# Optimization experiments

Hardware: AMD Instinct MI355X
Metric: run time of the kernel (lower is better)

## Reference

```python
import jax, jax.numpy as jnp
import numpy as np

THRESHOLD = 0.5
NEG_POS_RATIO = 3
ALPHA = 1.0
B, N_OBJ, N_PRIORS, N_CLASSES = 64, 32, 8732, 81


def xy_to_cxcy(xy):
    return jnp.concatenate([(xy[..., :2] + xy[..., 2:]) / 2.0, xy[..., 2:] - xy[..., :2]], axis=-1)


def cxcy_to_gcxgcy(cxcy, priors):
    return jnp.concatenate([
        (cxcy[..., :2] - priors[..., :2]) / (priors[..., 2:] / 10.0),
        jnp.log(cxcy[..., 2:] / priors[..., 2:]) * 5.0,
    ], axis=-1)


def jaccard(a, b):
    # a: [n,4], b: [m,4], both interpreted as (x1,y1,x2,y2) -- the original code
    # passes priors_cxcy directly (faithfully reproduced here).
    lt = jnp.maximum(a[:, None, :2], b[None, :, :2])
    rb = jnp.minimum(a[:, None, 2:], b[None, :, 2:])
    inter = jnp.prod(jnp.clip(rb - lt, 0.0, None), axis=-1)          # [n,m]
    area_a = jnp.prod(a[:, 2:] - a[:, :2], axis=-1)                  # [n]
    area_b = jnp.prod(b[:, 2:] - b[:, :2], axis=-1)                  # [m]
    return inter / (area_a[:, None] + area_b[None, :] - inter)


def _match(boxes_i, labels_i, priors_cxcy):
    # boxes_i: [n_obj,4] xy, labels_i: [n_obj] int, priors_cxcy: [n_priors,4]
    n_obj = boxes_i.shape[0]
    ov = jaccard(boxes_i, priors_cxcy)                               # [n_obj, n_priors]
    ov_for_prior = ov.max(axis=0)                                    # [n_priors]
    obj_for_prior = ov.argmax(axis=0)                                # [n_priors]
    prior_for_obj = ov.argmax(axis=1)                                # [n_obj]
    obj_for_prior = obj_for_prior.at[prior_for_obj].set(jnp.arange(n_obj))
    ov_for_prior = ov_for_prior.at[prior_for_obj].set(1.0)
    lab = labels_i[obj_for_prior]
    lab = jnp.where(ov_for_prior < THRESHOLD, 0, lab)                # background
    true_locs = cxcy_to_gcxgcy(xy_to_cxcy(boxes_i[obj_for_prior]), priors_cxcy)
    return true_locs, lab


def setup_inputs() -> dict:
    key = jax.random.key(0)
    k1, k2, k3, k4, k5, k6, k7 = jax.random.split(key, 7)
    predicted_locs = jax.random.normal(k1, (B, N_PRIORS, 4), dtype=jnp.float32)
    predicted_scores = jax.random.normal(k2, (B, N_PRIORS, N_CLASSES), dtype=jnp.float32)
    # valid gt boxes in xy form, inside [0,1]
    cxy = 0.15 + 0.7 * jax.random.uniform(k3, (B, N_OBJ, 2))
    wh = 0.05 + 0.25 * jax.random.uniform(k4, (B, N_OBJ, 2))
    boxes = jnp.clip(jnp.concatenate([cxy - wh / 2, cxy + wh / 2], axis=-1), 0.0, 1.0).astype(jnp.float32)
    labels = jax.random.randint(k5, (B, N_OBJ), 1, N_CLASSES)        # foreground classes
    # priors: cx,cy small, w,h large so that treating (cx,cy,w,h) as xy (as the
    # original code does in jaccard) still yields positive areas
    p_cxy = 0.4 * jax.random.uniform(k6, (N_PRIORS, 2))
    p_wh = 0.5 + 0.5 * jax.random.uniform(k7, (N_PRIORS, 2))
    priors_cxcy = jnp.concatenate([p_cxy, p_wh], axis=-1).astype(jnp.float32)
    return {
        "predicted_locs": predicted_locs,
        "predicted_scores": predicted_scores,
        "boxes": boxes,
        "labels": labels,
        "priors_cxcy": priors_cxcy,
    }


def multibox_loss(predicted_locs, predicted_scores, boxes, labels, priors_cxcy):
    n_priors = priors_cxcy.shape[0]
    true_locs, true_classes = jax.vmap(_match, in_axes=(0, 0, None))(boxes, labels, priors_cxcy)
    pos = true_classes != 0                                          # [B, n_priors]
    pos_f = pos.astype(predicted_locs.dtype)
    n_pos = pos.sum(axis=1)                                          # [B]
    n_pos_total = n_pos.sum().astype(jnp.float32)
    # nn.L1Loss(): mean over the 4 coords of positive priors
    loc_loss = (jnp.abs(predicted_locs - true_locs) * pos_f[..., None]).sum() / (n_pos_total * 4.0)
    # per-prior cross entropy
    logp = jax.nn.log_softmax(predicted_scores, axis=-1)             # [B,P,C]
    ce = -jnp.take_along_axis(logp, true_classes[..., None], axis=-1)[..., 0]  # [B,P]
    conf_pos = (ce * pos_f).sum()
    ce_neg = jnp.where(pos, 0.0, ce)
    ce_neg_sorted = -jnp.sort(-ce_neg, axis=1)                       # descending
    ranks = jnp.arange(n_priors)[None, :]
    hard = (ranks < (NEG_POS_RATIO * n_pos)[:, None]).astype(ce.dtype)
    conf_hard_neg = (ce_neg_sorted * hard).sum()
    conf_loss = (conf_hard_neg + conf_pos) / n_pos_total
    return conf_loss + ALPHA * loc_loss


def reference(predicted_locs, predicted_scores, boxes, labels, priors_cxcy):
    return multibox_loss(predicted_locs, predicted_scores, boxes, labels, priors_cxcy)
```

## Files before the change

kernel.cpp:

```cpp
#include <hip/hip_runtime.h>
#include <math.h>
#include <stdint.h>

#define BATCH 64
#define N_OBJ 32
#define NP 8732
#define NC 81
#define THRESH 0.5f


__device__ __forceinline__ float iou_box_prior(float x1, float y1, float x2, float y2,
                                               float areaA, float4 pr, float areaB) {
    float iw = fminf(x2, pr.z) - fmaxf(x1, pr.x); iw = fmaxf(iw, 0.f);
    float ih = fminf(y2, pr.w) - fmaxf(y1, pr.y); ih = fmaxf(ih, 0.f);
    float inter = iw * ih;
    return inter / (areaA + areaB - inter);
}

__global__ void k_match_prior(const float* __restrict__ boxes,
                              const float* __restrict__ priors,
                              float* __restrict__ ovp, int* __restrict__ objp,
                              int* __restrict__ n_pos, float* __restrict__ scal) {
    int i = blockIdx.y;
    int t = threadIdx.x;
    if (blockIdx.x == 0 && i == 0) {
        if (t < BATCH) n_pos[t] = 0;
        if (t < 3) scal[t] = 0.f;
    }
    __shared__ float bx[N_OBJ * 4];
    if (t < N_OBJ * 4) bx[t] = boxes[i * N_OBJ * 4 + t];
    __syncthreads();
    int p = blockIdx.x * blockDim.x + t;
    if (p >= NP) return;
    float4 pr = ((const float4*)priors)[p];
    float areaB = (pr.z - pr.x) * (pr.w - pr.y);
    float best = -1.0f; int bestj = 0;
    #pragma unroll
    for (int j = 0; j < N_OBJ; ++j) {
        float x1 = bx[j * 4 + 0], y1 = bx[j * 4 + 1], x2 = bx[j * 4 + 2], y2 = bx[j * 4 + 3];
        float areaA = (x2 - x1) * (y2 - y1);
        float v = iou_box_prior(x1, y1, x2, y2, areaA, pr, areaB);
        if (v > best) { best = v; bestj = j; }
    }
    ovp[i * NP + p] = best;
    objp[i * NP + p] = bestj;
}

__global__ void k_match_obj(const float* __restrict__ boxes,
                            const float* __restrict__ priors,
                            int* __restrict__ pfo) {
    int j = blockIdx.x, i = blockIdx.y;
    const float* bp = boxes + (i * N_OBJ + j) * 4;
    float x1 = bp[0], y1 = bp[1], x2 = bp[2], y2 = bp[3];
    float areaA = (x2 - x1) * (y2 - y1);
    float best = -1.f; int bestp = NP;
    for (int p = threadIdx.x; p < NP; p += blockDim.x) {
        float4 pr = ((const float4*)priors)[p];
        float areaB = (pr.z - pr.x) * (pr.w - pr.y);
        float v = iou_box_prior(x1, y1, x2, y2, areaA, pr, areaB);
        if (v > best) { best = v; bestp = p; }
    }
    __shared__ float sv[256];
    __shared__ int   si[256];
    int t = threadIdx.x;
    sv[t] = best; si[t] = bestp;
    __syncthreads();
    for (int s = 128; s > 0; s >>= 1) {
        if (t < s) {
            float v2 = sv[t + s]; int i2 = si[t + s];
            if (v2 > sv[t] || (v2 == sv[t] && i2 < si[t])) { sv[t] = v2; si[t] = i2; }
        }
        __syncthreads();
    }
    if (t == 0) pfo[i * N_OBJ + j] = si[0];
}

__global__ void k_force(const int* __restrict__ pfo,
                        float* __restrict__ ovp, int* __restrict__ objp) {
    int i = blockIdx.x * blockDim.x + threadIdx.x;
    if (i >= BATCH) return;
    for (int j = 0; j < N_OBJ; ++j) {
        int p = pfo[i * N_OBJ + j];
        objp[i * NP + p] = j;
        ovp[i * NP + p] = 1.0f;
    }
}

__global__ void __launch_bounds__(256)
k_ce(const float* __restrict__ scores,
     const float* __restrict__ plocs,
     const float* __restrict__ boxes,
     const int*   __restrict__ labels,
     const float* __restrict__ priors,
     const float* __restrict__ ovp,
     const int*   __restrict__ objp,
     float* __restrict__ ce_neg,
     int* __restrict__ n_pos, float* __restrict__ scal) {
    int i = blockIdx.y;
    int p = blockIdx.x * 256 + threadIdx.x;
    if (p >= NP) return;
    int gi = i * NP + p;

    int   obj = objp[gi];
    float ov  = ovp[gi];
    int   lab = (ov < THRESH) ? 0 : labels[i * N_OBJ + obj];

    const float* row = scores + (size_t)gi * NC;
    float slab = row[lab];

    float x[NC];
    #pragma unroll
    for (int e = 0; e < NC; ++e) x[e] = row[e];

    float m0 = x[0], m1 = x[1], m2 = x[2], m3 = x[3];
    #pragma unroll
    for (int e = 4; e + 3 < NC; e += 4) {
        m0 = fmaxf(m0, x[e + 0]);
        m1 = fmaxf(m1, x[e + 1]);
        m2 = fmaxf(m2, x[e + 2]);
        m3 = fmaxf(m3, x[e + 3]);
    }
    m0 = fmaxf(m0, x[NC - 1]);
    float m = fmaxf(fmaxf(m0, m1), fmaxf(m2, m3));

    float s0 = 0.f, s1 = 0.f, s2 = 0.f, s3 = 0.f;
    #pragma unroll
    for (int e = 0; e + 3 < NC; e += 4) {
        s0 += __expf(x[e + 0] - m);
        s1 += __expf(x[e + 1] - m);
        s2 += __expf(x[e + 2] - m);
        s3 += __expf(x[e + 3] - m);
    }
    s0 += __expf(x[NC - 1] - m);
    float s = (s0 + s1) + (s2 + s3);

    float lse = m + __logf(s);
    float ce = lse - slab;

    if (lab != 0) {
        atomicAdd(&n_pos[i], 1);
        atomicAdd(&scal[0], ce);
        const float* bp = boxes + (i * N_OBJ + obj) * 4;
        float bx1 = bp[0], by1 = bp[1], bx2 = bp[2], by2 = bp[3];
        float bcx = (bx1 + bx2) * 0.5f, bcy = (by1 + by2) * 0.5f;
        float bw = bx2 - bx1, bh = by2 - by1;
        float4 pr = ((const float4*)priors)[p];
        float g0 = (bcx - pr.x) / (pr.z / 10.0f);
        float g1 = (bcy - pr.y) / (pr.w / 10.0f);
        float g2 = logf(bw / pr.z) * 5.0f;
        float g3 = logf(bh / pr.w) * 5.0f;
        const float* pl = plocs + (size_t)gi * 4;
        float ll = fabsf(pl[0] - g0) + fabsf(pl[1] - g1)
                 + fabsf(pl[2] - g2) + fabsf(pl[3] - g3);
        atomicAdd(&scal[2], ll);
        ce_neg[gi] = 0.f;
    } else {
        ce_neg[gi] = ce;
    }
}

__global__ void __launch_bounds__(256)
k_topk(const float* __restrict__ ce_neg,
       const int* __restrict__ n_pos, float* __restrict__ scal) {
    int i = blockIdx.x;
    int t = threadIdx.x;
    float x[35];
    #pragma unroll
    for (int j = 0; j < 35; ++j) {
        int p = t + j * 256;
        x[j] = (p < NP) ? ce_neg[i * NP + p] : 0.f;
    }
    int k = 3 * n_pos[i];
    if (k > NP) k = NP;
    if (k <= 0) return;

    __shared__ int   cnt_s[4];
    __shared__ float sum_s[4];
    unsigned lo = 0u, hi = 0x7F800001u;
    while (hi - lo > 1u) {
        unsigned mid = lo + ((hi - lo) >> 1);
        int c = 0;
        #pragma unroll
        for (int j = 0; j < 35; ++j) c += (__float_as_uint(x[j]) >= mid) ? 1 : 0;
        #pragma unroll
        for (int off = 32; off; off >>= 1) c += __shfl_xor(c, off);
        if ((t & 63) == 0) cnt_s[t >> 6] = c;
        __syncthreads();
        int total = cnt_s[0] + cnt_s[1] + cnt_s[2] + cnt_s[3];
        __syncthreads();
        if (total >= k) lo = mid; else hi = mid;
    }
    float vk = __uint_as_float(lo);

    float s = 0.f; int c = 0;
    #pragma unroll
    for (int j = 0; j < 35; ++j) {
        float v = x[j];
        if (v > vk) { s += v; c++; }
    }
    #pragma unroll
    for (int off = 32; off; off >>= 1) { s += __shfl_xor(s, off); c += __shfl_xor(c, off); }
    if ((t & 63) == 0) { sum_s[t >> 6] = s; cnt_s[t >> 6] = c; }
    __syncthreads();
    if (t == 0) {
        float st = sum_s[0] + sum_s[1] + sum_s[2] + sum_s[3];
        int   ct = cnt_s[0] + cnt_s[1] + cnt_s[2] + cnt_s[3];
        atomicAdd(&scal[1], st + (float)(k - ct) * vk);
    }
}

__global__ void k_final(const int* __restrict__ n_pos,
                        const float* __restrict__ scal, float* __restrict__ out) {
    int t = threadIdx.x;
    int v = (t < BATCH) ? n_pos[t] : 0;
    #pragma unroll
    for (int off = 32; off; off >>= 1) v += __shfl_xor(v, off);
    if (t == 0) {
        float nf = (float)v;
        out[0] = (scal[1] + scal[0]) / nf + scal[2] / (nf * 4.0f);
    }
}

extern "C" void kernel_launch(void* const* d_in, const int* in_sizes, int n_in,
                              void* d_out, int out_size, void* d_ws, size_t ws_size,
                              hipStream_t stream) {
    const float* plocs  = (const float*)d_in[0];
    const float* scores = (const float*)d_in[1];
    const float* boxes  = (const float*)d_in[2];
    const int*   labels = (const int*)d_in[3];
    const float* priors = (const float*)d_in[4];
    float* out = (float*)d_out;

    char* ws = (char*)d_ws;
    size_t bp = (size_t)BATCH * NP * 4;
    float* ovp    = (float*)(ws);
    int*   objp   = (int*)  (ws + bp);
    float* ce_neg = (float*)(ws + 2 * bp);
    int*   pfo    = (int*)  (ws + 3 * bp);
    int*   n_pos  = pfo + BATCH * N_OBJ;
    float* scal   = (float*)(n_pos + BATCH);

    hipLaunchKernelGGL(k_match_prior, dim3((NP + 255) / 256, BATCH), dim3(256), 0, stream,
                       boxes, priors, ovp, objp, n_pos, scal);
    hipLaunchKernelGGL(k_match_obj, dim3(N_OBJ, BATCH), dim3(256), 0, stream,
                       boxes, priors, pfo);
    hipLaunchKernelGGL(k_force, dim3(1), dim3(64), 0, stream, pfo, ovp, objp);
    hipLaunchKernelGGL(k_ce, dim3((NP + 255) / 256, BATCH), dim3(256), 0, stream,
                       scores, plocs, boxes, labels, priors, ovp, objp, ce_neg, n_pos, scal);
    hipLaunchKernelGGL(k_topk, dim3(BATCH), dim3(256), 0, stream, ce_neg, n_pos, scal);
    hipLaunchKernelGGL(k_final, dim3(1), dim3(64), 0, stream, n_pos, scal, out);
}
```

Baseline: 188.7 us.

## Stream scores coalesced with wave segmented-scan row sums of exp

Replaces the per-thread strided read of each 81-class score row with a separate kernel that streams the whole score tensor as coalesced float4 loads. Each element is exponentiated, rows are summed with a wave-level segmented scan, and partial sums are combined with atomics into a per-row buffer. The later kernel then needs only log(rowsum) minus the label score. It also drops max subtraction in the log-sum-exp, which risks overflow for large logits, adds float atomics and makes the summation order non-deterministic.

After: 227.9 us. +20.8%, slower.

```diff
diff --git a/kernel.cpp b/kernel.cpp
--- a/kernel.cpp
+++ b/kernel.cpp
@@ -7,6 +7,9 @@
 #define NP 8732
 #define NC 81
 #define THRESH 0.5f
+#define NROWS (BATCH * NP)
+#define TOTAL4 ((BATCH * NP * NC) / 4)
+#define STRIDE4 (2048 * 256)
 
 
 __device__ __forceinline__ float iou_box_prior(float x1, float y1, float x2, float y2,
@@ -20,9 +23,12 @@
 __global__ void k_match_prior(const float* __restrict__ boxes,
                               const float* __restrict__ priors,
                               float* __restrict__ ovp, int* __restrict__ objp,
-                              int* __restrict__ n_pos, float* __restrict__ scal) {
+                              int* __restrict__ n_pos, float* __restrict__ scal,
+                              float* __restrict__ rowsum) {
     int i = blockIdx.y;
     int t = threadIdx.x;
+    int lin = (blockIdx.y * gridDim.x + blockIdx.x) * 256 + t;
+    if (lin < NROWS) rowsum[lin] = 0.f;
     if (blockIdx.x == 0 && i == 0) {
         if (t < BATCH) n_pos[t] = 0;
         if (t < 3) scal[t] = 0.f;
@@ -87,15 +93,71 @@
 }
 
 __global__ void __launch_bounds__(256)
-k_ce(const float* __restrict__ scores,
-     const float* __restrict__ plocs,
-     const float* __restrict__ boxes,
-     const int*   __restrict__ labels,
-     const float* __restrict__ priors,
-     const float* __restrict__ ovp,
-     const int*   __restrict__ objp,
-     float* __restrict__ ce_neg,
-     int* __restrict__ n_pos, float* __restrict__ scal) {
+k_sumexp(const float* __restrict__ scores, float* __restrict__ rowsum) {
+    int tid  = blockIdx.x * 256 + threadIdx.x;
+    int lane = threadIdx.x & 63;
+    const float4* s4 = (const float4*)scores;
+
+    #pragma unroll
+    for (int jb = 0; jb < 3; ++jb) {
+        const int NB = (jb < 2) ? 8 : 6;
+        float4 v[8];
+        #pragma unroll
+        for (int k = 0; k < 8; ++k) {
+            if (k < NB) {
+                int id = tid + (jb * 8 + k) * STRIDE4;
+                int idc = (id < TOTAL4) ? id : (TOTAL4 - 1);
+                v[k] = s4[idc];
+            }
+        }
+        #pragma unroll
+        for (int k = 0; k < 8; ++k) {
+            if (k >= NB) continue;
+            int id = tid + (jb * 8 + k) * STRIDE4;
+            float wt = (id < TOTAL4) ? 1.f : 0.f;
+            int idc = (id < TOTAL4) ? id : (TOTAL4 - 1);
+            int E = idc * 4;
+            unsigned r = (unsigned)E / 81u;
+            int rem = E - (int)(r * 81u);
+            float e0 = __expf(v[k].x), e1 = __expf(v[k].y);
+            float e2 = __expf(v[k].z), e3 = __expf(v[k].w);
+            int q = 81 - rem;
+            float s_lo, s_hi;
+            if (q >= 4)      { s_lo = (e0 + e1) + (e2 + e3); s_hi = 0.f; }
+            else if (q == 3) { s_lo = (e0 + e1) + e2;        s_hi = e3; }
+            else if (q == 2) { s_lo = e0 + e1;               s_hi = e2 + e3; }
+            else             { s_lo = e0;                    s_hi = (e1 + e2) + e3; }
+            s_lo *= wt; s_hi *= wt;
+
+            float sh = __shfl_up(s_hi, 1);
+            float x = s_lo + ((lane > 0) ? sh : 0.f);
+            if (lane == 63 && s_hi != 0.f) atomicAdd(&rowsum[r + 1], s_hi);
+
+            unsigned rr = r;
+            #pragma unroll
+            for (int off = 1; off < 64; off <<= 1) {
+                float    xv = __shfl_up(x, off);
+                unsigned kv = __shfl_up(rr, off);
+                if (lane >= off && kv == rr) x += xv;
+            }
+            unsigned rn = __shfl_down(rr, 1);
+            bool tail = (lane == 63) || (rn != rr);
+            if (tail && x != 0.f) atomicAdd(&rowsum[rr], x);
+        }
+    }
+}
+
+__global__ void __launch_bounds__(256)
+k_finish(const float* __restrict__ scores,
+         const float* __restrict__ plocs,
+         const float* __restrict__ boxes,
+         const int*   __restrict__ labels,
+         const float* __restrict__ priors,
+         const float* __restrict__ ovp,
+         const int*   __restrict__ objp,
+         const float* __restrict__ rowsum,
+         float* __restrict__ ce_neg,
+         int* __restrict__ n_pos, float* __restrict__ scal) {
     int i = blockIdx.y;
     int p = blockIdx.x * 256 + threadIdx.x;
     if (p >= NP) return;
@@ -104,38 +166,9 @@
     int   obj = objp[gi];
     float ov  = ovp[gi];
     int   lab = (ov < THRESH) ? 0 : labels[i * N_OBJ + obj];
-
-    const float* row = scores + (size_t)gi * NC;
-    float slab = row[lab];
-
-    float x[NC];
-    #pragma unroll
-    for (int e = 0; e < NC; ++e) x[e] = row[e];
-
-    float m0 = x[0], m1 = x[1], m2 = x[2], m3 = x[3];
-    #pragma unroll
-    for (int e = 4; e + 3 < NC; e += 4) {
-        m0 = fmaxf(m0, x[e + 0]);
-        m1 = fmaxf(m1, x[e + 1]);
-        m2 = fmaxf(m2, x[e + 2]);
-        m3 = fmaxf(m3, x[e + 3]);
-    }
-    m0 = fmaxf(m0, x[NC - 1]);
-    float m = fmaxf(fmaxf(m0, m1), fmaxf(m2, m3));
-
-    float s0 = 0.f, s1 = 0.f, s2 = 0.f, s3 = 0.f;
-    #pragma unroll
-    for (int e = 0; e + 3 < NC; e += 4) {
-        s0 += __expf(x[e + 0] - m);
-        s1 += __expf(x[e + 1] - m);
-        s2 += __expf(x[e + 2] - m);
-        s3 += __expf(x[e + 3] - m);
-    }
-    s0 += __expf(x[NC - 1] - m);
-    float s = (s0 + s1) + (s2 + s3);
-
-    float lse = m + __logf(s);
-    float ce = lse - slab;
+    float s    = rowsum[gi];
+    float slab = scores[(size_t)gi * NC + lab];
+    float ce = __logf(s) - slab;
 
     if (lab != 0) {
         atomicAdd(&n_pos[i], 1);
@@ -232,21 +265,24 @@
     float* out = (float*)d_out;
 
     char* ws = (char*)d_ws;
-    size_t bp = (size_t)BATCH * NP * 4;
+    size_t bp = (size_t)NROWS * 4;
     float* ovp    = (float*)(ws);
     int*   objp   = (int*)  (ws + bp);
     float* ce_neg = (float*)(ws + 2 * bp);
-    int*   pfo    = (int*)  (ws + 3 * bp);
+    float* rowsum = (float*)(ws + 3 * bp);
+    int*   pfo    = (int*)  (ws + 4 * bp);
     int*   n_pos  = pfo + BATCH * N_OBJ;
     float* scal   = (float*)(n_pos + BATCH);
 
     hipLaunchKernelGGL(k_match_prior, dim3((NP + 255) / 256, BATCH), dim3(256), 0, stream,
-                       boxes, priors, ovp, objp, n_pos, scal);
+                       boxes, priors, ovp, objp, n_pos, scal, rowsum);
+    hipLaunchKernelGGL(k_sumexp, dim3(2048), dim3(256), 0, stream, scores, rowsum);
     hipLaunchKernelGGL(k_match_obj, dim3(N_OBJ, BATCH), dim3(256), 0, stream,
                        boxes, priors, pfo);
     hipLaunchKernelGGL(k_force, dim3(1), dim3(64), 0, stream, pfo, ovp, objp);
-    hipLaunchKernelGGL(k_ce, dim3((NP + 255) / 256, BATCH), dim3(256), 0, stream,
-                       scores, plocs, boxes, labels, priors, ovp, objp, ce_neg, n_pos, scal);
+    hipLaunchKernelGGL(k_finish, dim3((NP + 255) / 256, BATCH), dim3(256), 0, stream,
+                       scores, plocs, boxes, labels, priors, ovp, objp, rowsum,
+                       ce_neg, n_pos, scal);
     hipLaunchKernelGGL(k_topk, dim3(BATCH), dim3(256), 0, stream, ce_neg, n_pos, scal);
     hipLaunchKernelGGL(k_final, dim3(1), dim3(64), 0, stream, n_pos, scal, out);
 }
```
